# Kernel optimization log

Hardware: AMD Instinct MI355X
Metric: run time of the kernel (lower is better)

Reference implementation:

```python
import jax, jax.numpy as jnp
import numpy as np

N = 100000      # nodes
E = 1600000     # edges (avg degree 16)
NF = 1          # node_feature_dim
EF = 1          # edge_feature_dim
H = 64          # hidden_dim
L = 5           # num_layers


def _linear_init(key, fan_in, fan_out):
    # torch nn.Linear default: U(-1/sqrt(fan_in), 1/sqrt(fan_in)) for W and b
    s = 1.0 / np.sqrt(fan_in)
    kw, kb = jax.random.split(key)
    w = jax.random.uniform(kw, (fan_in, fan_out), minval=-s, maxval=s, dtype=jnp.float32)
    b = jax.random.uniform(kb, (fan_out,), minval=-s, maxval=s, dtype=jnp.float32)
    return w, b


def setup_inputs() -> dict:
    key = jax.random.key(0)
    ks = jax.random.split(key, 8)
    x = jax.random.normal(ks[0], (N, NF), dtype=jnp.float32)
    edge_index = jax.random.randint(ks[1], (2, E), 0, N, dtype=jnp.int32)
    edge_attr = jax.random.uniform(ks[2], (E, EF), dtype=jnp.float32)

    emb_w, emb_b = _linear_init(ks[3], NF, H)
    fc_w, fc_b = _linear_init(ks[4], H, 1)

    msg_w1, msg_b1, msg_w2, msg_b2 = [], [], [], []
    upd_w1, upd_b1, upd_w2, upd_b2 = [], [], [], []
    lk = jax.random.split(ks[5], L)
    for l in range(L):
        k1, k2, k3, k4 = jax.random.split(lk[l], 4)
        w, b = _linear_init(k1, H + EF, H); msg_w1.append(w); msg_b1.append(b)
        w, b = _linear_init(k2, H, H);      msg_w2.append(w); msg_b2.append(b)
        w, b = _linear_init(k3, 2 * H, H);  upd_w1.append(w); upd_b1.append(b)
        w, b = _linear_init(k4, H, H);      upd_w2.append(w); upd_b2.append(b)

    stack = lambda xs: jnp.stack(xs, axis=0)
    return {
        "x": x, "edge_index": edge_index, "edge_attr": edge_attr,
        "emb_w": emb_w, "emb_b": emb_b,
        "msg_w1": stack(msg_w1), "msg_b1": stack(msg_b1),
        "msg_w2": stack(msg_w2), "msg_b2": stack(msg_b2),
        "upd_w1": stack(upd_w1), "upd_b1": stack(upd_b1),
        "upd_w2": stack(upd_w2), "upd_b2": stack(upd_b2),
        "fc_w": fc_w, "fc_b": fc_b,
    }


def reference(x, edge_index, edge_attr, emb_w, emb_b,
              msg_w1, msg_b1, msg_w2, msg_b2,
              upd_w1, upd_b1, upd_w2, upd_b2, fc_w, fc_b):
    src = edge_index[0]  # x_j (source)
    dst = edge_index[1]  # aggregation target i
    n = x.shape[0]

    h = x @ emb_w + emb_b  # [N, H]
    for l in range(msg_w1.shape[0]):
        # message: MLP(cat[x_j, edge_attr])
        m = jnp.concatenate([h[src], edge_attr], axis=1)  # [E, H+EF]
        m = jax.nn.relu(m @ msg_w1[l] + msg_b1[l]) @ msg_w2[l] + msg_b2[l]  # [E, H]
        # scatter-min aggregate; torch_scatter fills empty segments with 0
        aggr = jax.ops.segment_min(m, dst, num_segments=n)
        aggr = jnp.where(jnp.isfinite(aggr), aggr, jnp.zeros_like(aggr))
        # update: MLP(cat[x, aggr])
        u = jnp.concatenate([h, aggr], axis=1)  # [N, 2H]
        h = jax.nn.relu(u @ upd_w1[l] + upd_b1[l]) @ upd_w2[l] + upd_b2[l]
    return (h @ fc_w + fc_b).squeeze(-1)  # [N]
```

## Files before the change

### kernel.cpp

```cpp
#include <hip/hip_runtime.h>
#include <math.h>

#define N_NODES 100000
#define N_EDGES 1600000
#define HDIM 64
#define NBUCK 64
#define SCAN_T 1024
#define SCAN_CHUNK 98
#define NPB 128
#define LBLOCKS 782


__global__ __launch_bounds__(256) void k_zero_int(int* __restrict__ p, int n) {
  int i = blockIdx.x * 256 + threadIdx.x;
  if (i < n) p[i] = 0;
}

__global__ __launch_bounds__(256) void k_deg_count(const int* __restrict__ ei,
                                                   int* __restrict__ deg) {
  int e = blockIdx.x * 256 + threadIdx.x;
  if (e < N_EDGES) atomicAdd(&deg[ei[N_EDGES + e]], 1);
}

__global__ __launch_bounds__(SCAN_T) void k_rowptr(const int* __restrict__ deg,
                                                   int* __restrict__ row_ptr) {
  __shared__ int sums[SCAN_T];
  const int t = threadIdx.x;
  const int lo = t * SCAN_CHUNK;
  const int hi = min(lo + SCAN_CHUNK, N_NODES);
  int s = 0;
  for (int i = lo; i < hi; ++i) s += deg[i];
  sums[t] = s;
  __syncthreads();
  for (int off = 1; off < SCAN_T; off <<= 1) {
    int v = (t >= off) ? sums[t - off] : 0;
    __syncthreads();
    sums[t] += v;
    __syncthreads();
  }
  int run = (t == 0) ? 0 : sums[t - 1];
  for (int i = lo; i < hi; ++i) { row_ptr[i] = run; run += deg[i]; }
  if (t == SCAN_T - 1) row_ptr[N_NODES] = run;
}

__global__ __launch_bounds__(256) void k_scatter(
    const int* __restrict__ ei, const float* __restrict__ eattr,
    const int* __restrict__ row_ptr, int* __restrict__ cursor,
    int* __restrict__ s_src, float* __restrict__ s_ea) {
  int e = blockIdx.x * 256 + threadIdx.x;
  if (e >= N_EDGES) return;
  int d = ei[N_EDGES + e];
  int pos = row_ptr[d] + atomicAdd(&cursor[d], 1);
  s_src[pos] = ei[e];
  s_ea[pos] = eattr[e];
}

__global__ __launch_bounds__(256) void k_bucket_hist(const int* __restrict__ deg,
                                                     int* __restrict__ bhist) {
  int i = blockIdx.x * 256 + threadIdx.x;
  if (i < N_NODES) atomicAdd(&bhist[min(deg[i], NBUCK - 1)], 1);
}

__global__ __launch_bounds__(64) void k_bucket_scan(const int* __restrict__ bhist,
                                                    int* __restrict__ bcursor) {
  if (threadIdx.x == 0) {
    int run = 0;
    for (int b = 0; b < NBUCK; ++b) { bcursor[b] = run; run += bhist[b]; }
  }
}

__global__ __launch_bounds__(256) void k_bucket_scatter(const int* __restrict__ deg,
                                                        int* __restrict__ bcursor,
                                                        int* __restrict__ node_order) {
  __shared__ int lhist[NBUCK];
  __shared__ int lbase[NBUCK];
  __shared__ int lcur[NBUCK];
  const int t = threadIdx.x;
  const int i = blockIdx.x * 256 + t;
  if (t < NBUCK) { lhist[t] = 0; lcur[t] = 0; }
  __syncthreads();
  int b = -1;
  if (i < N_NODES) { b = min(deg[i], NBUCK - 1); atomicAdd(&lhist[b], 1); }
  __syncthreads();
  if (t < NBUCK && lhist[t] > 0) lbase[t] = atomicAdd(&bcursor[t], lhist[t]);
  __syncthreads();
  if (i < N_NODES) {
    int r = atomicAdd(&lcur[b], 1);
    node_order[lbase[b] + r] = i;
  }
}


__global__ __launch_bounds__(256) void k_embed_z(
    const float* __restrict__ x, const float* __restrict__ emb_w,
    const float* __restrict__ emb_b,
    const float* __restrict__ w1, const float* __restrict__ b1,
    float* __restrict__ h, float* __restrict__ z) {
  __shared__ float hs[64][65];
  const int t = threadIdx.x;
  const int nl = t >> 2;
  const int l4 = t & 3;
  const int i = blockIdx.x * 64 + nl;
  const bool valid = (i < N_NODES);
  const int jbase = l4 * 16;
  const float xv = valid ? x[i] : 0.0f;

  float hv[16];
  #pragma unroll
  for (int jj = 0; jj < 16; ++jj) {
    int j = jbase + jj;
    hv[jj] = fmaf(xv, emb_w[j], emb_b[j]);
    hs[nl][j] = hv[jj];
  }
  if (valid) {
    #pragma unroll
    for (int q = 0; q < 4; ++q)
      reinterpret_cast<float4*>(h + (size_t)i * HDIM)[l4 * 4 + q] =
          make_float4(hv[4*q], hv[4*q+1], hv[4*q+2], hv[4*q+3]);
  }
  __syncthreads();

  float acc[16];
  #pragma unroll
  for (int jj = 0; jj < 16; ++jj) acc[jj] = b1[jbase + jj];
  #pragma unroll 8
  for (int k = 0; k < 64; ++k) {
    float hk = hs[nl][k];
    const float* wr = w1 + k * 64 + jbase;
    #pragma unroll
    for (int jj = 0; jj < 16; ++jj) acc[jj] = fmaf(hk, wr[jj], acc[jj]);
  }
  if (valid) {
    #pragma unroll
    for (int q = 0; q < 4; ++q)
      reinterpret_cast<float4*>(z + (size_t)i * HDIM)[l4 * 4 + q] =
          make_float4(acc[4*q], acc[4*q+1], acc[4*q+2], acc[4*q+3]);
  }
}

template <int LAST>
__global__ __launch_bounds__(512) void k_layer(
    const int* __restrict__ node_order, const int* __restrict__ row_ptr,
    const int* __restrict__ s_src, const float* __restrict__ s_ea,
    const float* __restrict__ z_in,
    const float* __restrict__ w1b, const float* __restrict__ w2,
    const float* __restrict__ b2,
    const float* __restrict__ u1w, const float* __restrict__ u1b,
    const float* __restrict__ u2w, const float* __restrict__ u2b,
    const float* __restrict__ w1next, const float* __restrict__ b1next,
    const float* __restrict__ fcw, const float* __restrict__ fcb,
    float* __restrict__ h, float* __restrict__ z_out, float* __restrict__ out) {
  __shared__ float xch[NPB][65];
  __shared__ float ps[NPB][4];
  const int t = threadIdx.x;
  const int lane = t & 63;
  const int w = t >> 6;
  const int q  = __builtin_amdgcn_readfirstlane(w & 3);
  const int cw = __builtin_amdgcn_readfirstlane(w >> 2);
  const int jb = q * 16;
  const int nl = cw * 64 + lane;
  const int r = (LBLOCKS - 1 - (int)blockIdx.x) * NPB + nl;
  const bool valid = (r < N_NODES);
  const int node = valid ? node_order[r] : 0;
  const size_t hoff = (size_t)node * HDIM;

  float mn[16];
  #pragma unroll
  for (int j = 0; j < 16; ++j) mn[j] = INFINITY;

  if (valid) {
    const int p0 = row_ptr[node];
    const int p1 = row_ptr[node + 1];
    for (int p = p0; p < p1; ++p) {
      const int src = s_src[p];
      const float ea = s_ea[p];
      const float4* zr = reinterpret_cast<const float4*>(z_in + (size_t)src * HDIM);

      float m[16];
      #pragma unroll
      for (int j = 0; j < 16; ++j) m[j] = b2[jb + j];

      for (int k4 = 0; k4 < 16; ++k4) {
        float4 zv = zr[k4];
        float h0 = fmaxf(fmaf(ea, w1b[4*k4+0], zv.x), 0.0f);
        float h1 = fmaxf(fmaf(ea, w1b[4*k4+1], zv.y), 0.0f);
        float h2 = fmaxf(fmaf(ea, w1b[4*k4+2], zv.z), 0.0f);
        float h3 = fmaxf(fmaf(ea, w1b[4*k4+3], zv.w), 0.0f);
        const float* wr0 = w2 + (4*k4+0) * 64 + jb;
        const float* wr1 = w2 + (4*k4+1) * 64 + jb;
        const float* wr2 = w2 + (4*k4+2) * 64 + jb;
        const float* wr3 = w2 + (4*k4+3) * 64 + jb;
        #pragma unroll
        for (int j = 0; j < 16; ++j) m[j] = fmaf(h0, wr0[j], m[j]);
        #pragma unroll
        for (int j = 0; j < 16; ++j) m[j] = fmaf(h1, wr1[j], m[j]);
        #pragma unroll
        for (int j = 0; j < 16; ++j) m[j] = fmaf(h2, wr2[j], m[j]);
        #pragma unroll
        for (int j = 0; j < 16; ++j) m[j] = fmaf(h3, wr3[j], m[j]);
      }
      #pragma unroll
      for (int j = 0; j < 16; ++j) mn[j] = fminf(mn[j], m[j]);
    }
  }
  #pragma unroll
  for (int j = 0; j < 16; ++j)
    xch[nl][jb + j] = isinf(mn[j]) ? 0.0f : mn[j];
  __syncthreads();

  float acc[16];
  #pragma unroll
  for (int j = 0; j < 16; ++j) acc[j] = u1b[jb + j];
  {
    const float4* hr = reinterpret_cast<const float4*>(h + hoff);
    for (int k4 = 0; k4 < 16; ++k4) {
      float4 uv = hr[k4];
      const float* w0 = u1w + (4*k4+0) * 64 + jb;
      const float* w1 = u1w + (4*k4+1) * 64 + jb;
      const float* w2r = u1w + (4*k4+2) * 64 + jb;
      const float* w3 = u1w + (4*k4+3) * 64 + jb;
      #pragma unroll
      for (int j = 0; j < 16; ++j) acc[j] = fmaf(uv.x, w0[j], acc[j]);
      #pragma unroll
      for (int j = 0; j < 16; ++j) acc[j] = fmaf(uv.y, w1[j], acc[j]);
      #pragma unroll
      for (int j = 0; j < 16; ++j) acc[j] = fmaf(uv.z, w2r[j], acc[j]);
      #pragma unroll
      for (int j = 0; j < 16; ++j) acc[j] = fmaf(uv.w, w3[j], acc[j]);
    }
    for (int k = 0; k < 64; ++k) {
      float uk = xch[nl][k];
      const float* wr = u1w + (64 + k) * 64 + jb;
      #pragma unroll
      for (int j = 0; j < 16; ++j) acc[j] = fmaf(uk, wr[j], acc[j]);
    }
  }
  __syncthreads();
  #pragma unroll
  for (int j = 0; j < 16; ++j) xch[nl][jb + j] = fmaxf(acc[j], 0.0f);
  __syncthreads();

  float hn[16];
  #pragma unroll
  for (int j = 0; j < 16; ++j) hn[j] = u2b[jb + j];
  for (int k = 0; k < 64; ++k) {
    float hk = xch[nl][k];
    const float* wr = u2w + k * 64 + jb;
    #pragma unroll
    for (int j = 0; j < 16; ++j) hn[j] = fmaf(hk, wr[j], hn[j]);
  }
  if (valid) {
    #pragma unroll
    for (int v = 0; v < 4; ++v)
      reinterpret_cast<float4*>(h + hoff)[q * 4 + v] =
          make_float4(hn[4*v], hn[4*v+1], hn[4*v+2], hn[4*v+3]);
  }

  if (LAST) {
    float s = 0.0f;
    #pragma unroll
    for (int j = 0; j < 16; ++j) s = fmaf(hn[j], fcw[jb + j], s);
    ps[nl][q] = s;
    __syncthreads();
    if (q == 0 && valid)
      out[node] = ps[nl][0] + ps[nl][1] + ps[nl][2] + ps[nl][3] + fcb[0];
  } else {
    __syncthreads();
    #pragma unroll
    for (int j = 0; j < 16; ++j) xch[nl][jb + j] = hn[j];
    __syncthreads();
    float zz[16];
    #pragma unroll
    for (int j = 0; j < 16; ++j) zz[j] = b1next[jb + j];
    for (int k = 0; k < 64; ++k) {
      float hk = xch[nl][k];
      const float* wr = w1next + k * 64 + jb;
      #pragma unroll
      for (int j = 0; j < 16; ++j) zz[j] = fmaf(hk, wr[j], zz[j]);
    }
    if (valid) {
      #pragma unroll
      for (int v = 0; v < 4; ++v)
        reinterpret_cast<float4*>(z_out + hoff)[q * 4 + v] =
            make_float4(zz[4*v], zz[4*v+1], zz[4*v+2], zz[4*v+3]);
    }
  }
}

extern "C" void kernel_launch(void* const* d_in, const int* in_sizes, int n_in,
                              void* d_out, int out_size, void* d_ws, size_t ws_size,
                              hipStream_t stream) {
  const float* x      = (const float*)d_in[0];
  const int*   ei     = (const int*)d_in[1];
  const float* eattr  = (const float*)d_in[2];
  const float* emb_w  = (const float*)d_in[3];
  const float* emb_b  = (const float*)d_in[4];
  const float* msg_w1 = (const float*)d_in[5];
  const float* msg_b1 = (const float*)d_in[6];
  const float* msg_w2 = (const float*)d_in[7];
  const float* msg_b2 = (const float*)d_in[8];
  const float* upd_w1 = (const float*)d_in[9];
  const float* upd_b1 = (const float*)d_in[10];
  const float* upd_w2 = (const float*)d_in[11];
  const float* upd_b2 = (const float*)d_in[12];
  const float* fc_w   = (const float*)d_in[13];
  const float* fc_b   = (const float*)d_in[14];
  float* out = (float*)d_out;

  float* h     = (float*)d_ws;
  float* zA    = h + (size_t)N_NODES * HDIM;
  float* zB    = zA + (size_t)N_NODES * HDIM;
  float* s_ea  = zB + (size_t)N_NODES * HDIM;
  int*   s_src = (int*)(s_ea + N_EDGES);
  int*   row_ptr = s_src + N_EDGES;
  int*   node_order = row_ptr + (N_NODES + 1);
  int*   deg   = node_order + N_NODES;
  int*   cursor= deg + N_NODES;
  int*   bhist = cursor + N_NODES;
  int*   bcursor = bhist + NBUCK;

  const int nodeBlocks64 = (N_NODES + 63) / 64;
  const int nodeBlocks256 = (N_NODES + 255) / 256;
  const int edgeBlocks = (N_EDGES + 255) / 256;
  const int zeroN = 2 * N_NODES + NBUCK;

  k_zero_int<<<(zeroN + 255) / 256, 256, 0, stream>>>(deg, zeroN);
  k_deg_count<<<edgeBlocks, 256, 0, stream>>>(ei, deg);
  k_rowptr<<<1, SCAN_T, 0, stream>>>(deg, row_ptr);
  k_scatter<<<edgeBlocks, 256, 0, stream>>>(ei, eattr, row_ptr, cursor, s_src, s_ea);
  k_bucket_hist<<<nodeBlocks256, 256, 0, stream>>>(deg, bhist);
  k_bucket_scan<<<1, 64, 0, stream>>>(bhist, bcursor);
  k_bucket_scatter<<<nodeBlocks256, 256, 0, stream>>>(deg, bcursor, node_order);

  k_embed_z<<<nodeBlocks64, 256, 0, stream>>>(x, emb_w, emb_b, msg_w1, msg_b1, h, zA);

  float* zin = zA;
  float* zout = zB;
  for (int l = 0; l < 5; ++l) {
    const float* w1b = msg_w1 + l * 65 * 64 + 64 * 64;
    const float* w2  = msg_w2 + l * 64 * 64;
    const float* b2  = msg_b2 + l * 64;
    const float* u1w = upd_w1 + l * 128 * 64;
    const float* u1b = upd_b1 + l * 64;
    const float* u2w = upd_w2 + l * 64 * 64;
    const float* u2b = upd_b2 + l * 64;
    if (l < 4) {
      k_layer<0><<<LBLOCKS, 512, 0, stream>>>(
          node_order, row_ptr, s_src, s_ea, zin,
          w1b, w2, b2, u1w, u1b, u2w, u2b,
          msg_w1 + (l + 1) * 65 * 64, msg_b1 + (l + 1) * 64,
          nullptr, nullptr,
          h, zout, nullptr);
      float* tmp = zin; zin = zout; zout = tmp;
    } else {
      k_layer<1><<<LBLOCKS, 512, 0, stream>>>(
          node_order, row_ptr, s_src, s_ea, zin,
          w1b, w2, b2, u1w, u1b, u2w, u2b,
          nullptr, nullptr,
          fc_w, fc_b,
          h, nullptr, out);
    }
  }
}
```

Before: 2.688 ms.

## Switch message phase to edge-parallel per block with shared-memory atomicMin aggregation

```diff
diff --git a/kernel.cpp b/kernel.cpp
--- a/kernel.cpp
+++ b/kernel.cpp
@@ -4,11 +4,19 @@
 #define N_NODES 100000
 #define N_EDGES 1600000
 #define HDIM 64
-#define NBUCK 64
 #define SCAN_T 1024
 #define SCAN_CHUNK 98
 #define NPB 128
 #define LBLOCKS 782
+
+__device__ __forceinline__ unsigned encMin(float f) {
+  unsigned u = __float_as_uint(f);
+  return (u & 0x80000000u) ? ~u : (u | 0x80000000u);
+}
+__device__ __forceinline__ float decMin(unsigned u) {
+  unsigned b = (u & 0x80000000u) ? (u & 0x7FFFFFFFu) : ~u;
+  return __uint_as_float(b);
+}
 
 
 __global__ __launch_bounds__(256) void k_zero_int(int* __restrict__ p, int n) {
@@ -46,48 +54,14 @@
 __global__ __launch_bounds__(256) void k_scatter(
     const int* __restrict__ ei, const float* __restrict__ eattr,
     const int* __restrict__ row_ptr, int* __restrict__ cursor,
-    int* __restrict__ s_src, float* __restrict__ s_ea) {
+    int* __restrict__ s_src, float* __restrict__ s_ea, int* __restrict__ s_dl) {
   int e = blockIdx.x * 256 + threadIdx.x;
   if (e >= N_EDGES) return;
   int d = ei[N_EDGES + e];
   int pos = row_ptr[d] + atomicAdd(&cursor[d], 1);
   s_src[pos] = ei[e];
   s_ea[pos] = eattr[e];
-}
-
-__global__ __launch_bounds__(256) void k_bucket_hist(const int* __restrict__ deg,
-                                                     int* __restrict__ bhist) {
-  int i = blockIdx.x * 256 + threadIdx.x;
-  if (i < N_NODES) atomicAdd(&bhist[min(deg[i], NBUCK - 1)], 1);
-}
-
-__global__ __launch_bounds__(64) void k_bucket_scan(const int* __restrict__ bhist,
-                                                    int* __restrict__ bcursor) {
-  if (threadIdx.x == 0) {
-    int run = 0;
-    for (int b = 0; b < NBUCK; ++b) { bcursor[b] = run; run += bhist[b]; }
-  }
-}
-
-__global__ __launch_bounds__(256) void k_bucket_scatter(const int* __restrict__ deg,
-                                                        int* __restrict__ bcursor,
-                                                        int* __restrict__ node_order) {
-  __shared__ int lhist[NBUCK];
-  __shared__ int lbase[NBUCK];
-  __shared__ int lcur[NBUCK];
-  const int t = threadIdx.x;
-  const int i = blockIdx.x * 256 + t;
-  if (t < NBUCK) { lhist[t] = 0; lcur[t] = 0; }
-  __syncthreads();
-  int b = -1;
-  if (i < N_NODES) { b = min(deg[i], NBUCK - 1); atomicAdd(&lhist[b], 1); }
-  __syncthreads();
-  if (t < NBUCK && lhist[t] > 0) lbase[t] = atomicAdd(&bcursor[t], lhist[t]);
-  __syncthreads();
-  if (i < N_NODES) {
-    int r = atomicAdd(&lcur[b], 1);
-    node_order[lbase[b] + r] = i;
-  }
+  s_dl[pos] = d & (NPB - 1);
 }
 
 
@@ -139,9 +113,10 @@
 }
 
 template <int LAST>
-__global__ __launch_bounds__(512) void k_layer(
-    const int* __restrict__ node_order, const int* __restrict__ row_ptr,
+__global__ __launch_bounds__(256) void k_layer(
+    const int* __restrict__ row_ptr,
     const int* __restrict__ s_src, const float* __restrict__ s_ea,
+    const int* __restrict__ s_dl,
     const float* __restrict__ z_in,
     const float* __restrict__ w1b, const float* __restrict__ w2,
     const float* __restrict__ b2,
@@ -150,69 +125,115 @@
     const float* __restrict__ w1next, const float* __restrict__ b1next,
     const float* __restrict__ fcw, const float* __restrict__ fcb,
     float* __restrict__ h, float* __restrict__ z_out, float* __restrict__ out) {
-  __shared__ float xch[NPB][65];
-  __shared__ float ps[NPB][4];
+  __shared__ float hid_s[4][8][68];
+  __shared__ unsigned acc_u[NPB][65];
+  __shared__ float ps[NPB][2];
+  float* acc_f = (float*)acc_u;
+
   const int t = threadIdx.x;
   const int lane = t & 63;
-  const int w = t >> 6;
-  const int q  = __builtin_amdgcn_readfirstlane(w & 3);
-  const int cw = __builtin_amdgcn_readfirstlane(w >> 2);
-  const int jb = q * 16;
-  const int nl = cw * 64 + lane;
-  const int r = (LBLOCKS - 1 - (int)blockIdx.x) * NPB + nl;
-  const bool valid = (r < N_NODES);
-  const int node = valid ? node_order[r] : 0;
-  const size_t hoff = (size_t)node * HDIM;
-
-  float mn[16];
-  #pragma unroll
-  for (int j = 0; j < 16; ++j) mn[j] = INFINITY;
-
-  if (valid) {
-    const int p0 = row_ptr[node];
-    const int p1 = row_ptr[node + 1];
-    for (int p = p0; p < p1; ++p) {
-      const int src = s_src[p];
-      const float ea = s_ea[p];
-      const float4* zr = reinterpret_cast<const float4*>(z_in + (size_t)src * HDIM);
-
-      float m[16];
-      #pragma unroll
-      for (int j = 0; j < 16; ++j) m[j] = b2[jb + j];
-
-      for (int k4 = 0; k4 < 16; ++k4) {
-        float4 zv = zr[k4];
-        float h0 = fmaxf(fmaf(ea, w1b[4*k4+0], zv.x), 0.0f);
-        float h1 = fmaxf(fmaf(ea, w1b[4*k4+1], zv.y), 0.0f);
-        float h2 = fmaxf(fmaf(ea, w1b[4*k4+2], zv.z), 0.0f);
-        float h3 = fmaxf(fmaf(ea, w1b[4*k4+3], zv.w), 0.0f);
-        const float* wr0 = w2 + (4*k4+0) * 64 + jb;
-        const float* wr1 = w2 + (4*k4+1) * 64 + jb;
-        const float* wr2 = w2 + (4*k4+2) * 64 + jb;
-        const float* wr3 = w2 + (4*k4+3) * 64 + jb;
+  const int w = __builtin_amdgcn_readfirstlane(t >> 6);
+  const int nbase = blockIdx.x * NPB;
+
+  for (int i = t; i < NPB * 65; i += 256) ((unsigned*)acc_u)[i] = 0xFFFFFFFFu;
+  __syncthreads();
+
+  {
+    const int eb0 = row_ptr[nbase];
+    const int eb1 = row_ptr[min(nbase + NPB, N_NODES)];
+    const int n = eb1 - eb0;
+    const int we0 = eb0 + (n * w) / 4;
+    const int we1 = eb0 + (n * (w + 1)) / 4;
+
+    const int eL = lane >> 3;
+    const int q  = lane & 7;
+    const float4 w1bA = ((const float4*)w1b)[q];
+    const float4 w1bB = ((const float4*)w1b)[8 + q];
+    const float b2c = b2[lane];
+    float w2c[64];
+    #pragma unroll
+    for (int k = 0; k < 64; ++k) w2c[k] = w2[k * 64 + lane];
+
+    float run = INFINITY;
+    int cur = -1;
+
+    float4 ra, rb; float eaR = 0.0f;
+    ra = make_float4(0.f,0.f,0.f,0.f); rb = ra;
+    if (we0 + eL < we1) {
+      const int src = s_src[we0 + eL];
+      const float4* zr = (const float4*)(z_in + (size_t)src * HDIM);
+      ra = zr[q]; rb = zr[8 + q];
+      eaR = s_ea[we0 + eL];
+    }
+
+    for (int b = we0; b < we1; b += 8) {
+      float4 na = make_float4(0.f,0.f,0.f,0.f), nb = na; float ean = 0.0f;
+      if (b + 8 + eL < we1) {
+        const int srcn = s_src[b + 8 + eL];
+        const float4* zrn = (const float4*)(z_in + (size_t)srcn * HDIM);
+        na = zrn[q]; nb = zrn[8 + q];
+        ean = s_ea[b + 8 + eL];
+      }
+      if (b + eL < we1) {
+        float4 h0, h1;
+        h0.x = fmaxf(fmaf(eaR, w1bA.x, ra.x), 0.f);
+        h0.y = fmaxf(fmaf(eaR, w1bA.y, ra.y), 0.f);
+        h0.z = fmaxf(fmaf(eaR, w1bA.z, ra.z), 0.f);
+        h0.w = fmaxf(fmaf(eaR, w1bA.w, ra.w), 0.f);
+        h1.x = fmaxf(fmaf(eaR, w1bB.x, rb.x), 0.f);
+        h1.y = fmaxf(fmaf(eaR, w1bB.y, rb.y), 0.f);
+        h1.z = fmaxf(fmaf(eaR, w1bB.z, rb.z), 0.f);
+        h1.w = fmaxf(fmaf(eaR, w1bB.w, rb.w), 0.f);
+        *(float4*)&hid_s[w][eL][q * 4] = h0;
+        *(float4*)&hid_s[w][eL][32 + q * 4] = h1;
+      }
+      #pragma unroll
+      for (int e2 = 0; e2 < 8; ++e2) {
+        if (b + e2 >= we1) break;
+        float m0 = b2c, m1 = 0.f, m2 = 0.f, m3 = 0.f;
         #pragma unroll
-        for (int j = 0; j < 16; ++j) m[j] = fmaf(h0, wr0[j], m[j]);
-        #pragma unroll
-        for (int j = 0; j < 16; ++j) m[j] = fmaf(h1, wr1[j], m[j]);
-        #pragma unroll
-        for (int j = 0; j < 16; ++j) m[j] = fmaf(h2, wr2[j], m[j]);
-        #pragma unroll
-        for (int j = 0; j < 16; ++j) m[j] = fmaf(h3, wr3[j], m[j]);
+        for (int k4 = 0; k4 < 16; ++k4) {
+          float4 hq = *(const float4*)&hid_s[w][e2][k4 * 4];
+          m0 = fmaf(hq.x, w2c[4*k4+0], m0);
+          m1 = fmaf(hq.y, w2c[4*k4+1], m1);
+          m2 = fmaf(hq.z, w2c[4*k4+2], m2);
+          m3 = fmaf(hq.w, w2c[4*k4+3], m3);
+        }
+        float m = (m0 + m1) + (m2 + m3);
+        const int dl = s_dl[b + e2];
+        if (dl != cur) {
+          if (cur >= 0) atomicMin(&acc_u[cur][lane], encMin(run));
+          cur = dl; run = INFINITY;
+        }
+        run = fminf(run, m);
       }
-      #pragma unroll
-      for (int j = 0; j < 16; ++j) mn[j] = fminf(mn[j], m[j]);
-    }
-  }
-  #pragma unroll
-  for (int j = 0; j < 16; ++j)
-    xch[nl][jb + j] = isinf(mn[j]) ? 0.0f : mn[j];
-  __syncthreads();
-
-  float acc[16];
-  #pragma unroll
-  for (int j = 0; j < 16; ++j) acc[j] = u1b[jb + j];
+      ra = na; rb = nb; eaR = ean;
+    }
+    if (cur >= 0) atomicMin(&acc_u[cur][lane], encMin(run));
+  }
+  __syncthreads();
+
+  const int half = w & 1;
+  const int pr = w >> 1;
+  const int jb = half * 32;
+  const int nl = pr * 64 + lane;
+  const int node = nbase + nl;
+  const bool valid = (node < N_NODES);
+  const size_t off = (size_t)(valid ? node : 0) * HDIM;
+
+  #pragma unroll
+  for (int j = 0; j < 32; ++j) {
+    float f = decMin(acc_u[nl][jb + j]);
+    if (!isfinite(f)) f = 0.f;
+    acc_f[nl * 65 + jb + j] = f;
+  }
+  __syncthreads();
+
+  float acc[32];
+  #pragma unroll
+  for (int j = 0; j < 32; ++j) acc[j] = u1b[jb + j];
   {
-    const float4* hr = reinterpret_cast<const float4*>(h + hoff);
+    const float4* hr = reinterpret_cast<const float4*>(h + off);
     for (int k4 = 0; k4 < 16; ++k4) {
       float4 uv = hr[k4];
       const float* w0 = u1w + (4*k4+0) * 64 + jb;
@@ -220,68 +241,70 @@
       const float* w2r = u1w + (4*k4+2) * 64 + jb;
       const float* w3 = u1w + (4*k4+3) * 64 + jb;
       #pragma unroll
-      for (int j = 0; j < 16; ++j) acc[j] = fmaf(uv.x, w0[j], acc[j]);
-      #pragma unroll
-      for (int j = 0; j < 16; ++j) acc[j] = fmaf(uv.y, w1[j], acc[j]);
-      #pragma unroll
-      for (int j = 0; j < 16; ++j) acc[j] = fmaf(uv.z, w2r[j], acc[j]);
-      #pragma unroll
-      for (int j = 0; j < 16; ++j) acc[j] = fmaf(uv.w, w3[j], acc[j]);
-    }
+      for (int j = 0; j < 32; ++j) acc[j] = fmaf(uv.x, w0[j], acc[j]);
+      #pragma unroll
+      for (int j = 0; j < 32; ++j) acc[j] = fmaf(uv.y, w1[j], acc[j]);
+      #pragma unroll
+      for (int j = 0; j < 32; ++j) acc[j] = fmaf(uv.z, w2r[j], acc[j]);
+      #pragma unroll
+      for (int j = 0; j < 32; ++j) acc[j] = fmaf(uv.w, w3[j], acc[j]);
+    }
+    #pragma unroll 4
     for (int k = 0; k < 64; ++k) {
-      float uk = xch[nl][k];
+      float uk = acc_f[nl * 65 + k];
       const float* wr = u1w + (64 + k) * 64 + jb;
       #pragma unroll
-      for (int j = 0; j < 16; ++j) acc[j] = fmaf(uk, wr[j], acc[j]);
-    }
-  }
-  __syncthreads();
-  #pragma unroll
-  for (int j = 0; j < 16; ++j) xch[nl][jb + j] = fmaxf(acc[j], 0.0f);
-  __syncthreads();
-
-  float hn[16];
-  #pragma unroll
-  for (int j = 0; j < 16; ++j) hn[j] = u2b[jb + j];
+      for (int j = 0; j < 32; ++j) acc[j] = fmaf(uk, wr[j], acc[j]);
+    }
+  }
+  __syncthreads();
+  #pragma unroll
+  for (int j = 0; j < 32; ++j) acc_f[nl * 65 + jb + j] = fmaxf(acc[j], 0.f);
+  __syncthreads();
+
+  float hn[32];
+  #pragma unroll
+  for (int j = 0; j < 32; ++j) hn[j] = u2b[jb + j];
+  #pragma unroll 4
   for (int k = 0; k < 64; ++k) {
-    float hk = xch[nl][k];
+    float hk = acc_f[nl * 65 + k];
     const float* wr = u2w + k * 64 + jb;
     #pragma unroll
-    for (int j = 0; j < 16; ++j) hn[j] = fmaf(hk, wr[j], hn[j]);
+    for (int j = 0; j < 32; ++j) hn[j] = fmaf(hk, wr[j], hn[j]);
   }
   if (valid) {
     #pragma unroll
-    for (int v = 0; v < 4; ++v)
-      reinterpret_cast<float4*>(h + hoff)[q * 4 + v] =
+    for (int v = 0; v < 8; ++v)
+      reinterpret_cast<float4*>(h + off)[half * 8 + v] =
           make_float4(hn[4*v], hn[4*v+1], hn[4*v+2], hn[4*v+3]);
   }
 
   if (LAST) {
     float s = 0.0f;
     #pragma unroll
-    for (int j = 0; j < 16; ++j) s = fmaf(hn[j], fcw[jb + j], s);
-    ps[nl][q] = s;
-    __syncthreads();
-    if (q == 0 && valid)
-      out[node] = ps[nl][0] + ps[nl][1] + ps[nl][2] + ps[nl][3] + fcb[0];
+    for (int j = 0; j < 32; ++j) s = fmaf(hn[j], fcw[jb + j], s);
+    ps[nl][half] = s;
+    __syncthreads();
+    if (half == 0 && valid) out[node] = ps[nl][0] + ps[nl][1] + fcb[0];
   } else {
     __syncthreads();
     #pragma unroll
-    for (int j = 0; j < 16; ++j) xch[nl][jb + j] = hn[j];
-    __syncthreads();
-    float zz[16];
-    #pragma unroll
-    for (int j = 0; j < 16; ++j) zz[j] = b1next[jb + j];
+    for (int j = 0; j < 32; ++j) acc_f[nl * 65 + jb + j] = hn[j];
+    __syncthreads();
+    float zz[32];
+    #pragma unroll
+    for (int j = 0; j < 32; ++j) zz[j] = b1next[jb + j];
+    #pragma unroll 4
     for (int k = 0; k < 64; ++k) {
-      float hk = xch[nl][k];
+      float hk = acc_f[nl * 65 + k];
       const float* wr = w1next + k * 64 + jb;
       #pragma unroll
-      for (int j = 0; j < 16; ++j) zz[j] = fmaf(hk, wr[j], zz[j]);
+      for (int j = 0; j < 32; ++j) zz[j] = fmaf(hk, wr[j], zz[j]);
     }
     if (valid) {
       #pragma unroll
-      for (int v = 0; v < 4; ++v)
-        reinterpret_cast<float4*>(z_out + hoff)[q * 4 + v] =
+      for (int v = 0; v < 8; ++v)
+        reinterpret_cast<float4*>(z_out + off)[half * 8 + v] =
             make_float4(zz[4*v], zz[4*v+1], zz[4*v+2], zz[4*v+3]);
     }
   }
@@ -312,25 +335,19 @@
   float* zB    = zA + (size_t)N_NODES * HDIM;
   float* s_ea  = zB + (size_t)N_NODES * HDIM;
   int*   s_src = (int*)(s_ea + N_EDGES);
-  int*   row_ptr = s_src + N_EDGES;
-  int*   node_order = row_ptr + (N_NODES + 1);
-  int*   deg   = node_order + N_NODES;
+  int*   s_dl  = s_src + N_EDGES;
+  int*   row_ptr = s_dl + N_EDGES;
+  int*   deg   = row_ptr + (N_NODES + 1);
   int*   cursor= deg + N_NODES;
-  int*   bhist = cursor + N_NODES;
-  int*   bcursor = bhist + NBUCK;
 
   const int nodeBlocks64 = (N_NODES + 63) / 64;
-  const int nodeBlocks256 = (N_NODES + 255) / 256;
   const int edgeBlocks = (N_EDGES + 255) / 256;
-  const int zeroN = 2 * N_NODES + NBUCK;
-
-  k_zero_int<<<(zeroN + 255) / 256, 256, 0, stream>>>(deg, zeroN);
+
+  k_zero_int<<<(2 * N_NODES + 255) / 256, 256, 0, stream>>>(deg, 2 * N_NODES);
   k_deg_count<<<edgeBlocks, 256, 0, stream>>>(ei, deg);
   k_rowptr<<<1, SCAN_T, 0, stream>>>(deg, row_ptr);
-  k_scatter<<<edgeBlocks, 256, 0, stream>>>(ei, eattr, row_ptr, cursor, s_src, s_ea);
-  k_bucket_hist<<<nodeBlocks256, 256, 0, stream>>>(deg, bhist);
-  k_bucket_scan<<<1, 64, 0, stream>>>(bhist, bcursor);
-  k_bucket_scatter<<<nodeBlocks256, 256, 0, stream>>>(deg, bcursor, node_order);
+  k_scatter<<<edgeBlocks, 256, 0, stream>>>(ei, eattr, row_ptr, cursor,
+                                            s_src, s_ea, s_dl);
 
   k_embed_z<<<nodeBlocks64, 256, 0, stream>>>(x, emb_w, emb_b, msg_w1, msg_b1, h, zA);
 
@@ -345,16 +362,16 @@
     const float* u2w = upd_w2 + l * 64 * 64;
     const float* u2b = upd_b2 + l * 64;
     if (l < 4) {
-      k_layer<0><<<LBLOCKS, 512, 0, stream>>>(
-          node_order, row_ptr, s_src, s_ea, zin,
+      k_layer<0><<<LBLOCKS, 256, 0, stream>>>(
+          row_ptr, s_src, s_ea, s_dl, zin,
           w1b, w2, b2, u1w, u1b, u2w, u2b,
           msg_w1 + (l + 1) * 65 * 64, msg_b1 + (l + 1) * 64,
           nullptr, nullptr,
           h, zout, nullptr);
       float* tmp = zin; zin = zout; zout = tmp;
     } else {
-      k_layer<1><<<LBLOCKS, 512, 0, stream>>>(
-          node_order, row_ptr, s_src, s_ea, zin,
+      k_layer<1><<<LBLOCKS, 256, 0, stream>>>(
+          row_ptr, s_src, s_ea, s_dl, zin,
           w1b, w2, b2, u1w, u1b, u2w, u2b,
           nullptr, nullptr,
           fc_w, fc_b,
```

Result: faster. 2.560 ms (-4.8%).
